# Kernel tuning notes

Measured on AMD Instinct MI355X. Metric: run time of the kernel, lower is better.

Reference implementation:

```python
import jax, jax.numpy as jnp
import numpy as np

EPS = 1e-5

def _layernorm(x, gamma, beta):
    mu = jnp.mean(x, axis=-1, keepdims=True)
    var = jnp.var(x, axis=-1, keepdims=True)
    return (x - mu) * jax.lax.rsqrt(var + EPS) * gamma + beta

def setup_inputs() -> dict:
    key = jax.random.key(0)
    ks = jax.random.split(key, 8)
    B, N, c_z, c_h = 1, 384, 128, 128
    s_z = 1.0 / np.sqrt(c_z)
    s_h = 1.0 / np.sqrt(c_h)
    return {
        "z_ij": jax.random.normal(ks[0], (B, N, N, c_z), dtype=jnp.float32),
        "ln_in_g": jnp.ones((c_z,), jnp.float32),
        "ln_in_b": jnp.zeros((c_z,), jnp.float32),
        "ln_out_g": jnp.ones((c_h,), jnp.float32),
        "ln_out_b": jnp.zeros((c_h,), jnp.float32),
        "Wa1": jax.random.uniform(ks[1], (c_h, c_z), jnp.float32, -s_z, s_z),
        "Wa2": jax.random.uniform(ks[2], (c_h, c_z), jnp.float32, -s_z, s_z),
        "Wb1": jax.random.uniform(ks[3], (c_h, c_z), jnp.float32, -s_z, s_z),
        "Wb2": jax.random.uniform(ks[4], (c_h, c_z), jnp.float32, -s_z, s_z),
        "Wg": jax.random.uniform(ks[5], (c_z, c_z), jnp.float32, -s_z, s_z),
        "Wout": jax.random.uniform(ks[6], (c_z, c_h), jnp.float32, -s_h, s_h),
    }

def reference(z_ij, ln_in_g, ln_in_b, ln_out_g, ln_out_b, Wa1, Wa2, Wb1, Wb2, Wg, Wout):
    # Algorithm 12: triangular multiplicative update, "outgoing" edges
    z = _layernorm(z_ij, ln_in_g, ln_in_b)              # [B,N,N,c_z]
    a = jax.nn.sigmoid(z @ Wa1.T) * (z @ Wa2.T)         # [B,N,N,c_h]
    b = jax.nn.sigmoid(z @ Wb1.T) * (z @ Wb2.T)         # [B,N,N,c_h]
    g = jax.nn.sigmoid(z @ Wg.T)                        # [B,N,N,c_z]
    s = jnp.einsum('bikd,bjkd->bijd', a, b)             # pairwise contraction over k
    return g * (_layernorm(s, ln_out_g, ln_out_b) @ Wout.T)
```

## Files before the change

kernel.cpp:

```cpp
#include <hip/hip_runtime.h>
#include <stdint.h>

#define N 384
#define NR (N*N)
#define PL (NR + 64)
#define C 128
#define WSZ 16384

typedef unsigned short ushort_t;
typedef __attribute__((ext_vector_type(8))) _Float16 f16x8;
typedef __attribute__((ext_vector_type(4))) float f32x4;

__device__ __forceinline__ ushort_t f2h(float f) {
  union { _Float16 h; ushort_t u; } v; v.h = (_Float16)f; return v.u;
}
__device__ __forceinline__ float h2f(ushort_t u) {
  union { _Float16 h; ushort_t u; } v; v.u = u; return (float)v.h;
}
__device__ __forceinline__ void unpack8h(uint4 q, float f[8]) {
  union { uint4 q; _Float16 h[8]; } v; v.q = q;
#pragma unroll
  for (int e = 0; e < 8; ++e) f[e] = (float)v.h[e];
}
__device__ __forceinline__ uint4 pack8h(const float f[8]) {
  union { uint4 q; _Float16 h[8]; } v;
#pragma unroll
  for (int e = 0; e < 8; ++e) v.h[e] = (_Float16)f[e];
  return v.q;
}

__device__ __forceinline__ float bf2f(ushort_t u) {
  union { unsigned int i; float f; } v; v.i = ((unsigned int)u) << 16; return v.f;
}
__device__ __forceinline__ ushort_t f2bf(float f) {
  union { float f; unsigned int i; } v; v.f = f;
  unsigned int u = v.i + 0x7FFF + ((v.i >> 16) & 1);
  return (ushort_t)(u >> 16);
}
__device__ __forceinline__ void unpack8bf(uint4 q, float f[8]) {
  const unsigned int* w = (const unsigned int*)&q;
#pragma unroll
  for (int e = 0; e < 4; ++e) {
    f[2*e]   = bf2f((ushort_t)(w[e] & 0xffffu));
    f[2*e+1] = bf2f((ushort_t)(w[e] >> 16));
  }
}
__device__ __forceinline__ uint4 pack8bf(const float f[8]) {
  uint4 q;
  unsigned int* w = (unsigned int*)&q;
#pragma unroll
  for (int e = 0; e < 4; ++e)
    w[e] = (unsigned int)f2bf(f[2*e]) | ((unsigned int)f2bf(f[2*e+1]) << 16);
  return q;
}

__device__ __forceinline__ float sigmoidf_(float x) {
  return __builtin_amdgcn_rcpf(1.0f + __expf(-x));
}

__device__ __forceinline__ void load8f(const void* p, size_t idx, int isf32, float f[8]) {
  if (isf32) {
    const float* q = (const float*)p + idx;
    const float4 a = ((const float4*)q)[0];
    const float4 b = ((const float4*)q)[1];
    f[0]=a.x; f[1]=a.y; f[2]=a.z; f[3]=a.w;
    f[4]=b.x; f[5]=b.y; f[6]=b.z; f[7]=b.w;
  } else {
    unpack8bf(*(const uint4*)((const ushort_t*)p + idx), f);
  }
}
__device__ __forceinline__ void store8(void* p, size_t idx, int isf32, const float f[8]) {
  if (isf32) {
    float* q = (float*)p + idx;
    ((float4*)q)[0] = make_float4(f[0], f[1], f[2], f[3]);
    ((float4*)q)[1] = make_float4(f[4], f[5], f[6], f[7]);
  } else {
    *(uint4*)((ushort_t*)p + idx) = pack8bf(f);
  }
}
__device__ __forceinline__ void store1(void* p, size_t idx, int isf32, float v) {
  if (isf32) ((float*)p)[idx] = v;
  else       ((ushort_t*)p)[idx] = f2bf(v);
}

__global__ void kprep(const unsigned int* __restrict__ zw,
                      const void* __restrict__ Wa1, const void* __restrict__ Wa2,
                      const void* __restrict__ Wb1, const void* __restrict__ Wb2,
                      const void* __restrict__ Wg,  const void* __restrict__ Wout,
                      ushort_t* __restrict__ wp, int* __restrict__ flag)
{
  const int t = threadIdx.x;
  __shared__ int cnt[4];
  {
    unsigned int u = zw[t];
    int e = (u >> 23) & 0xFF;
    int sane = (e >= 87 && e <= 132) ? 1 : 0;
    unsigned long long b = __ballot(sane);
    if ((t & 63) == 0) cnt[t >> 6] = __popcll(b);
  }
  __syncthreads();
  const int isf32 = ((cnt[0] + cnt[1] + cnt[2] + cnt[3]) >= 128) ? 1 : 0;
  if (blockIdx.x == 0 && t == 0) flag[0] = isf32;

  const void* src;
  switch (blockIdx.x) {
    case 0: src = Wa1; break;
    case 1: src = Wa2; break;
    case 2: src = Wb1; break;
    case 3: src = Wb2; break;
    case 4: src = Wg;  break;
    default: src = Wout; break;
  }
  ushort_t* dst = wp + (size_t)blockIdx.x * WSZ;
  for (int c = t; c < 2048; c += 256) {
    int ks = c >> 9, nf = (c >> 6) & 7, lane = c & 63;
    int quad = lane >> 4, l16 = lane & 15;
    size_t sidx = (size_t)(nf*16 + l16)*128 + ks*32 + quad*8;
    float f[8]; load8f(src, sidx, isf32, f);
    *(uint4*)(dst + (size_t)c*8) = pack8h(f);
  }
}

__global__ __launch_bounds__(256, 2)
void k1(const void* __restrict__ z, const void* __restrict__ gin,
        const void* __restrict__ bin, const ushort_t* __restrict__ wp,
        ushort_t* __restrict__ a_t, ushort_t* __restrict__ b_t,
        void* __restrict__ gout, ushort_t* __restrict__ g_t, int gIsWs,
        const int* __restrict__ flag)
{
  __shared__ ushort_t tb[128*72];
  const int t = threadIdx.x;
  const int isf32 = *flag;
  const int wave = t >> 6, lane = t & 63;
  const int quad = lane >> 4, l16 = lane & 15;
  const int rg = wave >> 1, ch = wave & 1;
  const int R0 = blockIdx.x * 64;
  const f32x4 z4 = {0.f, 0.f, 0.f, 0.f};

  f16x8 af[2][4];
#pragma unroll
  for (int mf = 0; mf < 2; ++mf) {
    const int row = R0 + rg*32 + mf*16 + l16;
    f16x8 xh[4];
    float s = 0.f, q = 0.f;
#pragma unroll
    for (int ks = 0; ks < 4; ++ks) {
      float x[8];
      load8f(z, (size_t)row*C + ks*32 + quad*8, isf32, x);
      union { _Float16 h[8]; f16x8 v; } u;
#pragma unroll
      for (int e = 0; e < 8; ++e) {
        s += x[e]; q += x[e]*x[e];
        u.h[e] = (_Float16)x[e];
      }
      xh[ks] = u.v;
    }
    s += __shfl_xor(s, 16); s += __shfl_xor(s, 32);
    q += __shfl_xor(q, 16); q += __shfl_xor(q, 32);
    const float mu = s * 0.0078125f;
    const float rstd = rsqrtf(q * 0.0078125f - mu*mu + 1e-5f);
#pragma unroll
    for (int ks = 0; ks < 4; ++ks) {
      float ga[8], be[8];
      load8f(gin, (size_t)(ks*32 + quad*8), isf32, ga);
      load8f(bin, (size_t)(ks*32 + quad*8), isf32, be);
      union { _Float16 h[8]; f16x8 v; } xi; xi.v = xh[ks];
      union { alignas(16) _Float16 h[8]; f16x8 v; } u;
#pragma unroll
      for (int e = 0; e < 8; ++e)
        u.h[e] = (_Float16)(((float)xi.h[e] - mu) * rstd * ga[e] + be[e]);
      af[mf][ks] = u.v;
    }
  }

  auto pair = [&](const ushort_t* W1p, const ushort_t* W2p, ushort_t* dst) {
#pragma unroll 1
    for (int nh = 0; nh < 2; ++nh) {
      f32x4 a1[2][2], a2[2][2];
#pragma unroll
      for (int mf = 0; mf < 2; ++mf)
#pragma unroll
        for (int nn = 0; nn < 2; ++nn) { a1[mf][nn] = z4; a2[mf][nn] = z4; }
#pragma unroll
      for (int ks = 0; ks < 4; ++ks)
#pragma unroll
        for (int nn = 0; nn < 2; ++nn) {
          const size_t foff = (size_t)((ks*8 + ch*4 + nh*2 + nn)*64 + lane) * 8;
          f16x8 b1 = *(const f16x8*)(W1p + foff);
          f16x8 b2 = *(const f16x8*)(W2p + foff);
#pragma unroll
          for (int mf = 0; mf < 2; ++mf) {
            a1[mf][nn] = __builtin_amdgcn_mfma_f32_16x16x32_f16(af[mf][ks], b1, a1[mf][nn], 0, 0, 0);
            a2[mf][nn] = __builtin_amdgcn_mfma_f32_16x16x32_f16(af[mf][ks], b2, a2[mf][nn], 0, 0, 0);
          }
        }
#pragma unroll
      for (int mf = 0; mf < 2; ++mf)
#pragma unroll
        for (int nn = 0; nn < 2; ++nn)
#pragma unroll
          for (int r = 0; r < 4; ++r) {
            int rowl = rg*32 + mf*16 + quad*4 + r;
            int col  = ch*64 + (nh*2 + nn)*16 + l16;
            tb[col*72 + rowl] = f2h(a2[mf][nn][r] * sigmoidf_(a1[mf][nn][r]));
          }
    }
    asm volatile("s_waitcnt lgkmcnt(0)" ::: "memory");
    __builtin_amdgcn_s_barrier();
#pragma unroll
    for (int i = 0; i < 4; ++i) {
      int cid = t + i*256, dl = cid >> 3, rc = cid & 7;
      uint4 v = *(const uint4*)(tb + dl*72 + rc*8);
      *(uint4*)(dst + (size_t)dl*PL + R0 + rc*8) = v;
    }
    asm volatile("" ::: "memory");
    __builtin_amdgcn_s_barrier();
  };
  pair(wp + 0*WSZ, wp + 1*WSZ, a_t);
  pair(wp + 2*WSZ, wp + 3*WSZ, b_t);

  {
    const ushort_t* Wgp = wp + 4*WSZ;
    f32x4 ag[2][4];
#pragma unroll
    for (int mf = 0; mf < 2; ++mf)
#pragma unroll
      for (int nf = 0; nf < 4; ++nf) ag[mf][nf] = z4;
#pragma unroll
    for (int ks = 0; ks < 4; ++ks)
#pragma unroll
      for (int nf = 0; nf < 4; ++nf) {
        const size_t foff = (size_t)((ks*8 + ch*4 + nf)*64 + lane) * 8;
        f16x8 b = *(const f16x8*)(Wgp + foff);
#pragma unroll
        for (int mf = 0; mf < 2; ++mf)
          ag[mf][nf] = __builtin_amdgcn_mfma_f32_16x16x32_f16(af[mf][ks], b, ag[mf][nf], 0, 0, 0);
      }
#pragma unroll
    for (int mf = 0; mf < 2; ++mf)
#pragma unroll
      for (int nf = 0; nf < 4; ++nf)
#pragma unroll
        for (int r = 0; r < 4; ++r) {
          int row = R0 + rg*32 + mf*16 + quad*4 + r;
          int col = ch*64 + nf*16 + l16;
          float v = sigmoidf_(ag[mf][nf][r]);
          size_t idx = (size_t)row*C + col;
          if (gIsWs) g_t[idx] = f2h(v);
          else       store1(gout, idx, isf32, v);
        }
  }
}

__global__ __launch_bounds__(256, 3)
void k2(const ushort_t* __restrict__ a_t, const ushort_t* __restrict__ b_t,
        ushort_t* __restrict__ s_t)
{
  __shared__ ushort_t As[128*64];
  __shared__ ushort_t Bs[128*64];
  const int t = threadIdx.x;
  const int wave = t >> 6, lane = t & 63;
  const int quad = lane >> 4, l16 = lane & 15;
  const int wm = wave >> 1, wn = wave & 1;
  const int lin = blockIdx.x;
  const int xcd = lin & 7, slot = lin >> 3;
  const int d = xcd + 8*(slot/9);
  const int tile = slot - (slot/9)*9;
  const int i0 = (tile/3) * 128, j0 = (tile%3) * 128;
  const size_t dbase = (size_t)d * PL;

  f32x4 acc[4][4];
  const f32x4 z4 = {0.f, 0.f, 0.f, 0.f};
#pragma unroll
  for (int mf = 0; mf < 4; ++mf)
#pragma unroll
    for (int nf = 0; nf < 4; ++nf) acc[mf][nf] = z4;

  uint4 va[4], vb[4];
#pragma unroll
  for (int j = 0; j < 4; ++j) {
    int cid = t + j*256, row = cid >> 3, c = cid & 7;
    va[j] = *(const uint4*)(a_t + dbase + (size_t)(i0 + row)*N + c*8);
    vb[j] = *(const uint4*)(b_t + dbase + (size_t)(j0 + row)*N + c*8);
  }

  for (int kt = 0; kt < 6; ++kt) {
#pragma unroll
    for (int j = 0; j < 4; ++j) {
      int cid = t + j*256, row = cid >> 3, c = cid & 7;
      int p = c ^ (row & 7);
      *(uint4*)(As + row*64 + p*8) = va[j];
      *(uint4*)(Bs + row*64 + p*8) = vb[j];
    }
    if (kt < 5) {
#pragma unroll
      for (int j = 0; j < 4; ++j) {
        int cid = t + j*256, row = cid >> 3, c = cid & 7;
        va[j] = *(const uint4*)(a_t + dbase + (size_t)(i0 + row)*N + (kt+1)*64 + c*8);
        vb[j] = *(const uint4*)(b_t + dbase + (size_t)(j0 + row)*N + (kt+1)*64 + c*8);
      }
    }
    asm volatile("s_waitcnt lgkmcnt(0)" ::: "memory");
    __builtin_amdgcn_s_barrier();

#pragma unroll
    for (int ks = 0; ks < 2; ++ks) {
      f16x8 af[4], bfr[4];
#pragma unroll
      for (int f = 0; f < 4; ++f) {
        int ra = wm*64 + f*16 + l16;
        int pa = (ks*4 + quad) ^ (ra & 7);
        af[f] = *(const f16x8*)(As + ra*64 + pa*8);
        int rb = wn*64 + f*16 + l16;
        int pb = (ks*4 + quad) ^ (rb & 7);
        bfr[f] = *(const f16x8*)(Bs + rb*64 + pb*8);
      }
#pragma unroll
      for (int mf = 0; mf < 4; ++mf)
#pragma unroll
        for (int nf = 0; nf < 4; ++nf)
          acc[mf][nf] = __builtin_amdgcn_mfma_f32_16x16x32_f16(af[mf], bfr[nf], acc[mf][nf], 0, 0, 0);
    }
    asm volatile("" ::: "memory");
    __builtin_amdgcn_s_barrier();
  }
#pragma unroll
  for (int mf = 0; mf < 4; ++mf)
#pragma unroll
    for (int nf = 0; nf < 4; ++nf)
#pragma unroll
      for (int r = 0; r < 4; ++r) {
        int row = wm*64 + mf*16 + quad*4 + r;
        int col = wn*64 + nf*16 + l16;
        s_t[dbase + (size_t)(i0 + row)*N + j0 + col] = f2h(acc[mf][nf][r]);
      }
}

__global__ __launch_bounds__(256, 2)
void k3(const ushort_t* __restrict__ s_t, const void* __restrict__ gno,
        const void* __restrict__ bno, const ushort_t* __restrict__ wp,
        void* __restrict__ io, const ushort_t* __restrict__ g_t, int gIsWs,
        const int* __restrict__ flag)
{
  __shared__ ushort_t ss[128*136];
  const int t = threadIdx.x;
  const int isf32 = *flag;
  const int wave = t >> 6, lane = t & 63;
  const int quad = lane >> 4, l16 = lane & 15;
  const int R0 = blockIdx.x * 128;
  const ushort_t* Woutp = wp + 5*WSZ;

  {
    const int dg = t >> 4, rg = t & 15;
    const int d0 = dg * 8;
    uint4 v[8];
#pragma unroll
    for (int dd = 0; dd < 8; ++dd)
      v[dd] = *(const uint4*)(s_t + (size_t)(d0 + dd)*PL + R0 + rg*8);
    const ushort_t* sv = (const ushort_t*)v;
#pragma unroll
    for (int rr0 = 0; rr0 < 8; ++rr0) {
      int rr = (rr0 + (t & 7)) & 7;
      ushort_t w[8];
#pragma unroll
      for (int dd = 0; dd < 8; ++dd) w[dd] = sv[dd*8 + rr];
      *(uint4*)(ss + (rg*8 + rr)*136 + d0) = *(const uint4*)w;
    }
  }
  asm volatile("s_waitcnt lgkmcnt(0)" ::: "memory");
  __builtin_amdgcn_s_barrier();

  {
    const int r = t >> 1, h = t & 1;
    float sum = 0.f, sq = 0.f;
#pragma unroll
    for (int j = 0; j < 8; ++j) {
      uint4 q = *(const uint4*)(ss + r*136 + (h*8 + j)*8);
      float f[8]; unpack8h(q, f);
#pragma unroll
      for (int e = 0; e < 8; ++e) { sum += f[e]; sq += f[e]*f[e]; }
    }
    sum += __shfl_xor(sum, 1);
    sq  += __shfl_xor(sq, 1);
    const float mu = sum * 0.0078125f;
    const float rstd = rsqrtf(sq * 0.0078125f - mu*mu + 1e-5f);
#pragma unroll
    for (int j = 0; j < 8; ++j) {
      const int g = h*8 + j;
      uint4 q = *(const uint4*)(ss + r*136 + g*8);
      float f[8], gm[8], bt[8];
      unpack8h(q, f);
      load8f(gno, (size_t)g*8, isf32, gm);
      load8f(bno, (size_t)g*8, isf32, bt);
#pragma unroll
      for (int e = 0; e < 8; ++e) f[e] = (f[e] - mu) * rstd * gm[e] + bt[e];
      *(uint4*)(ss + r*136 + g*8) = pack8h(f);
    }
  }
  asm volatile("s_waitcnt lgkmcnt(0)" ::: "memory");
  __builtin_amdgcn_s_barrier();

  f16x8 afr[2][4];
#pragma unroll
  for (int ks = 0; ks < 4; ++ks)
#pragma unroll
    for (int mf = 0; mf < 2; ++mf) {
      int row = wave*32 + mf*16 + l16;
      afr[mf][ks] = *(const f16x8*)(ss + row*136 + (ks*4 + quad)*8);
    }
  asm volatile("s_waitcnt lgkmcnt(0)" ::: "memory");
  __builtin_amdgcn_s_barrier();

  const f32x4 z4 = {0.f, 0.f, 0.f, 0.f};
#pragma unroll 1
  for (int nh = 0; nh < 2; ++nh) {
    f32x4 acc[2][4];
#pragma unroll
    for (int mf = 0; mf < 2; ++mf)
#pragma unroll
      for (int nn = 0; nn < 4; ++nn) acc[mf][nn] = z4;
#pragma unroll
    for (int ks = 0; ks < 4; ++ks)
#pragma unroll
      for (int nn = 0; nn < 4; ++nn) {
        size_t foff = (size_t)(((ks*8 + nh*4 + nn)*64 + lane)) * 8;
        f16x8 b = *(const f16x8*)(Woutp + foff);
#pragma unroll
        for (int mf = 0; mf < 2; ++mf)
          acc[mf][nn] = __builtin_amdgcn_mfma_f32_16x16x32_f16(afr[mf][ks], b, acc[mf][nn], 0, 0, 0);
      }
#pragma unroll
    for (int mf = 0; mf < 2; ++mf)
#pragma unroll
      for (int nn = 0; nn < 4; ++nn)
#pragma unroll
        for (int r = 0; r < 4; ++r) {
          int row = wave*32 + mf*16 + quad*4 + r;
          int col = (nh*4 + nn)*16 + l16;
          ss[row*136 + col] = f2h(acc[mf][nn][r]);
        }
  }
  asm volatile("s_waitcnt lgkmcnt(0)" ::: "memory");
  __builtin_amdgcn_s_barrier();

#pragma unroll
  for (int i = 0; i < 8; ++i) {
    int cid = t + i*256;
    int row = cid >> 4, ch = cid & 15;
    size_t idx = (size_t)(R0 + row)*C + ch*8;
    float gf[8], hf[8], of[8];
    if (gIsWs) unpack8h(*(const uint4*)(g_t + idx), gf);
    else       load8f(io, idx, isf32, gf);
    unpack8h(*(const uint4*)(ss + row*136 + ch*8), hf);
#pragma unroll
    for (int e = 0; e < 8; ++e) of[e] = gf[e] * hf[e];
    store8(io, idx, isf32, of);
  }
}

extern "C" void kernel_launch(void* const* d_in, const int* in_sizes, int n_in,
                              void* d_out, int out_size, void* d_ws, size_t ws_size,
                              hipStream_t stream) {
  (void)in_sizes; (void)n_in; (void)out_size;
  const void* z    = d_in[0];
  const void* gin  = d_in[1];
  const void* bin  = d_in[2];
  const void* gno  = d_in[3];
  const void* bno  = d_in[4];
  const void* Wa1  = d_in[5];
  const void* Wa2  = d_in[6];
  const void* Wb1  = d_in[7];
  const void* Wb2  = d_in[8];
  const void* Wg   = d_in[9];
  const void* Wout = d_in[10];

  const size_t plane = (size_t)C * PL;
  int* flag     = (int*)d_ws;
  ushort_t* wp  = (ushort_t*)((char*)d_ws + 256);
  ushort_t* a_t = wp + (size_t)6*WSZ;
  ushort_t* b_t = a_t + plane;
  ushort_t* s_t = b_t + plane;
  ushort_t* g_t = s_t + plane;
  size_t need_g = 256 + (size_t)6*WSZ*2 + (3*plane + (size_t)NR*C)*2;
  int gIsWs = (ws_size >= need_g) ? 1 : 0;

  kprep<<<6, 256, 0, stream>>>((const unsigned int*)z, Wa1, Wa2, Wb1, Wb2, Wg, Wout, wp, flag);
  k1<<<NR/64, 256, 0, stream>>>(z, gin, bin, wp, a_t, b_t, d_out, g_t, gIsWs, flag);
  k2<<<1152, 256, 0, stream>>>(a_t, b_t, s_t);
  k3<<<NR/128, 256, 0, stream>>>(s_t, gno, bno, wp, d_out, g_t, gIsWs, flag);
}
```

Measured before the change: 323.9 us.

## Double-buffer LDS in pairwise GEMM and cut register pressure in projection kernel

The contraction kernel now keeps two LDS buffers for the A and B tiles, so the next k-tile is written to the other buffer while MFMAs run on the current one. This removes one barrier per k-iteration. The doubled shared memory forces the occupancy hint down from 3 to 2 blocks per CU. In the projection kernel, the fp16 copy of the input row is no longer held in registers; the input is re-read from global memory to normalize it, which also avoids an extra fp16 rounding before normalization. The gate and pair GEMMs now loop over one output fragment at a time, shrinking the live accumulator set.

```diff
diff --git a/kernel.cpp b/kernel.cpp
--- a/kernel.cpp
+++ b/kernel.cpp
@@ -141,19 +141,13 @@
 #pragma unroll
   for (int mf = 0; mf < 2; ++mf) {
     const int row = R0 + rg*32 + mf*16 + l16;
-    f16x8 xh[4];
     float s = 0.f, q = 0.f;
 #pragma unroll
     for (int ks = 0; ks < 4; ++ks) {
       float x[8];
       load8f(z, (size_t)row*C + ks*32 + quad*8, isf32, x);
-      union { _Float16 h[8]; f16x8 v; } u;
-#pragma unroll
-      for (int e = 0; e < 8; ++e) {
-        s += x[e]; q += x[e]*x[e];
-        u.h[e] = (_Float16)x[e];
-      }
-      xh[ks] = u.v;
+#pragma unroll
+      for (int e = 0; e < 8; ++e) { s += x[e]; q += x[e]*x[e]; }
     }
     s += __shfl_xor(s, 16); s += __shfl_xor(s, 32);
     q += __shfl_xor(q, 16); q += __shfl_xor(q, 32);
@@ -161,49 +155,42 @@
     const float rstd = rsqrtf(q * 0.0078125f - mu*mu + 1e-5f);
 #pragma unroll
     for (int ks = 0; ks < 4; ++ks) {
-      float ga[8], be[8];
+      float x[8], ga[8], be[8];
+      load8f(z, (size_t)row*C + ks*32 + quad*8, isf32, x);
       load8f(gin, (size_t)(ks*32 + quad*8), isf32, ga);
       load8f(bin, (size_t)(ks*32 + quad*8), isf32, be);
-      union { _Float16 h[8]; f16x8 v; } xi; xi.v = xh[ks];
       union { alignas(16) _Float16 h[8]; f16x8 v; } u;
 #pragma unroll
       for (int e = 0; e < 8; ++e)
-        u.h[e] = (_Float16)(((float)xi.h[e] - mu) * rstd * ga[e] + be[e]);
+        u.h[e] = (_Float16)((x[e] - mu) * rstd * ga[e] + be[e]);
       af[mf][ks] = u.v;
     }
   }
 
   auto pair = [&](const ushort_t* W1p, const ushort_t* W2p, ushort_t* dst) {
 #pragma unroll 1
-    for (int nh = 0; nh < 2; ++nh) {
-      f32x4 a1[2][2], a2[2][2];
+    for (int nf = 0; nf < 4; ++nf) {
+      f32x4 a1[2], a2[2];
+      a1[0] = z4; a1[1] = z4; a2[0] = z4; a2[1] = z4;
+#pragma unroll
+      for (int ks = 0; ks < 4; ++ks) {
+        const size_t foff = (size_t)((ks*8 + ch*4 + nf)*64 + lane) * 8;
+        f16x8 b1 = *(const f16x8*)(W1p + foff);
+        f16x8 b2 = *(const f16x8*)(W2p + foff);
+#pragma unroll
+        for (int mf = 0; mf < 2; ++mf) {
+          a1[mf] = __builtin_amdgcn_mfma_f32_16x16x32_f16(af[mf][ks], b1, a1[mf], 0, 0, 0);
+          a2[mf] = __builtin_amdgcn_mfma_f32_16x16x32_f16(af[mf][ks], b2, a2[mf], 0, 0, 0);
+        }
+      }
 #pragma unroll
       for (int mf = 0; mf < 2; ++mf)
 #pragma unroll
-        for (int nn = 0; nn < 2; ++nn) { a1[mf][nn] = z4; a2[mf][nn] = z4; }
-#pragma unroll
-      for (int ks = 0; ks < 4; ++ks)
-#pragma unroll
-        for (int nn = 0; nn < 2; ++nn) {
-          const size_t foff = (size_t)((ks*8 + ch*4 + nh*2 + nn)*64 + lane) * 8;
-          f16x8 b1 = *(const f16x8*)(W1p + foff);
-          f16x8 b2 = *(const f16x8*)(W2p + foff);
-#pragma unroll
-          for (int mf = 0; mf < 2; ++mf) {
-            a1[mf][nn] = __builtin_amdgcn_mfma_f32_16x16x32_f16(af[mf][ks], b1, a1[mf][nn], 0, 0, 0);
-            a2[mf][nn] = __builtin_amdgcn_mfma_f32_16x16x32_f16(af[mf][ks], b2, a2[mf][nn], 0, 0, 0);
-          }
+        for (int r = 0; r < 4; ++r) {
+          int rowl = rg*32 + mf*16 + quad*4 + r;
+          int col  = ch*64 + nf*16 + l16;
+          tb[col*72 + rowl] = f2h(a2[mf][r] * sigmoidf_(a1[mf][r]));
         }
-#pragma unroll
-      for (int mf = 0; mf < 2; ++mf)
-#pragma unroll
-        for (int nn = 0; nn < 2; ++nn)
-#pragma unroll
-          for (int r = 0; r < 4; ++r) {
-            int rowl = rg*32 + mf*16 + quad*4 + r;
-            int col  = ch*64 + (nh*2 + nn)*16 + l16;
-            tb[col*72 + rowl] = f2h(a2[mf][nn][r] * sigmoidf_(a1[mf][nn][r]));
-          }
     }
     asm volatile("s_waitcnt lgkmcnt(0)" ::: "memory");
     __builtin_amdgcn_s_barrier();
@@ -221,43 +208,39 @@
 
   {
     const ushort_t* Wgp = wp + 4*WSZ;
-    f32x4 ag[2][4];
-#pragma unroll
-    for (int mf = 0; mf < 2; ++mf)
-#pragma unroll
-      for (int nf = 0; nf < 4; ++nf) ag[mf][nf] = z4;
-#pragma unroll
-    for (int ks = 0; ks < 4; ++ks)
-#pragma unroll
-      for (int nf = 0; nf < 4; ++nf) {
+#pragma unroll 1
+    for (int nf = 0; nf < 4; ++nf) {
+      f32x4 ag[2];
+      ag[0] = z4; ag[1] = z4;
+#pragma unroll
+      for (int ks = 0; ks < 4; ++ks) {
         const size_t foff = (size_t)((ks*8 + ch*4 + nf)*64 + lane) * 8;
         f16x8 b = *(const f16x8*)(Wgp + foff);
 #pragma unroll
         for (int mf = 0; mf < 2; ++mf)
-          ag[mf][nf] = __builtin_amdgcn_mfma_f32_16x16x32_f16(af[mf][ks], b, ag[mf][nf], 0, 0, 0);
-      }
-#pragma unroll
-    for (int mf = 0; mf < 2; ++mf)
-#pragma unroll
-      for (int nf = 0; nf < 4; ++nf)
+          ag[mf] = __builtin_amdgcn_mfma_f32_16x16x32_f16(af[mf][ks], b, ag[mf], 0, 0, 0);
+      }
+#pragma unroll
+      for (int mf = 0; mf < 2; ++mf)
 #pragma unroll
         for (int r = 0; r < 4; ++r) {
           int row = R0 + rg*32 + mf*16 + quad*4 + r;
           int col = ch*64 + nf*16 + l16;
-          float v = sigmoidf_(ag[mf][nf][r]);
+          float v = sigmoidf_(ag[mf][r]);
           size_t idx = (size_t)row*C + col;
           if (gIsWs) g_t[idx] = f2h(v);
           else       store1(gout, idx, isf32, v);
         }
-  }
-}
-
-__global__ __launch_bounds__(256, 3)
+    }
+  }
+}
+
+__global__ __launch_bounds__(256, 2)
 void k2(const ushort_t* __restrict__ a_t, const ushort_t* __restrict__ b_t,
         ushort_t* __restrict__ s_t)
 {
-  __shared__ ushort_t As[128*64];
-  __shared__ ushort_t Bs[128*64];
+  __shared__ ushort_t As[2][128*64];
+  __shared__ ushort_t Bs[2][128*64];
   const int t = threadIdx.x;
   const int wave = t >> 6, lane = t & 63;
   const int quad = lane >> 4, l16 = lane & 15;
@@ -283,46 +266,65 @@
     va[j] = *(const uint4*)(a_t + dbase + (size_t)(i0 + row)*N + c*8);
     vb[j] = *(const uint4*)(b_t + dbase + (size_t)(j0 + row)*N + c*8);
   }
+#pragma unroll
+  for (int j = 0; j < 4; ++j) {
+    int cid = t + j*256, row = cid >> 3, c = cid & 7;
+    int p = c ^ (row & 7);
+    *(uint4*)(&As[0][0] + row*64 + p*8) = va[j];
+    *(uint4*)(&Bs[0][0] + row*64 + p*8) = vb[j];
+  }
+#pragma unroll
+  for (int j = 0; j < 4; ++j) {
+    int cid = t + j*256, row = cid >> 3, c = cid & 7;
+    va[j] = *(const uint4*)(a_t + dbase + (size_t)(i0 + row)*N + 64 + c*8);
+    vb[j] = *(const uint4*)(b_t + dbase + (size_t)(j0 + row)*N + 64 + c*8);
+  }
+  asm volatile("s_waitcnt lgkmcnt(0)" ::: "memory");
+  __builtin_amdgcn_s_barrier();
 
   for (int kt = 0; kt < 6; ++kt) {
-#pragma unroll
-    for (int j = 0; j < 4; ++j) {
-      int cid = t + j*256, row = cid >> 3, c = cid & 7;
-      int p = c ^ (row & 7);
-      *(uint4*)(As + row*64 + p*8) = va[j];
-      *(uint4*)(Bs + row*64 + p*8) = vb[j];
-    }
-    if (kt < 5) {
-#pragma unroll
-      for (int j = 0; j < 4; ++j) {
-        int cid = t + j*256, row = cid >> 3, c = cid & 7;
-        va[j] = *(const uint4*)(a_t + dbase + (size_t)(i0 + row)*N + (kt+1)*64 + c*8);
-        vb[j] = *(const uint4*)(b_t + dbase + (size_t)(j0 + row)*N + (kt+1)*64 + c*8);
-      }
-    }
-    asm volatile("s_waitcnt lgkmcnt(0)" ::: "memory");
-    __builtin_amdgcn_s_barrier();
-
+    const int cur = kt & 1;
+    const ushort_t* Ab = &As[cur][0];
+    const ushort_t* Bb = &Bs[cur][0];
 #pragma unroll
     for (int ks = 0; ks < 2; ++ks) {
-      f16x8 af[4], bfr[4];
+      f16x8 afr[4], bfr[4];
 #pragma unroll
       for (int f = 0; f < 4; ++f) {
         int ra = wm*64 + f*16 + l16;
         int pa = (ks*4 + quad) ^ (ra & 7);
-        af[f] = *(const f16x8*)(As + ra*64 + pa*8);
+        afr[f] = *(const f16x8*)(Ab + ra*64 + pa*8);
         int rb = wn*64 + f*16 + l16;
         int pb = (ks*4 + quad) ^ (rb & 7);
-        bfr[f] = *(const f16x8*)(Bs + rb*64 + pb*8);
+        bfr[f] = *(const f16x8*)(Bb + rb*64 + pb*8);
       }
 #pragma unroll
       for (int mf = 0; mf < 4; ++mf)
 #pragma unroll
         for (int nf = 0; nf < 4; ++nf)
-          acc[mf][nf] = __builtin_amdgcn_mfma_f32_16x16x32_f16(af[mf], bfr[nf], acc[mf][nf], 0, 0, 0);
-    }
-    asm volatile("" ::: "memory");
-    __builtin_amdgcn_s_barrier();
+          acc[mf][nf] = __builtin_amdgcn_mfma_f32_16x16x32_f16(afr[mf], bfr[nf], acc[mf][nf], 0, 0, 0);
+    }
+    if (kt < 5) {
+      ushort_t* Aw = &As[cur ^ 1][0];
+      ushort_t* Bw = &Bs[cur ^ 1][0];
+#pragma unroll
+      for (int j = 0; j < 4; ++j) {
+        int cid = t + j*256, row = cid >> 3, c = cid & 7;
+        int p = c ^ (row & 7);
+        *(uint4*)(Aw + row*64 + p*8) = va[j];
+        *(uint4*)(Bw + row*64 + p*8) = vb[j];
+      }
+      if (kt < 4) {
+#pragma unroll
+        for (int j = 0; j < 4; ++j) {
+          int cid = t + j*256, row = cid >> 3, c = cid & 7;
+          va[j] = *(const uint4*)(a_t + dbase + (size_t)(i0 + row)*N + (kt+2)*64 + c*8);
+          vb[j] = *(const uint4*)(b_t + dbase + (size_t)(j0 + row)*N + (kt+2)*64 + c*8);
+        }
+      }
+      asm volatile("s_waitcnt lgkmcnt(0)" ::: "memory");
+      __builtin_amdgcn_s_barrier();
+    }
   }
 #pragma unroll
   for (int mf = 0; mf < 4; ++mf)
```

Measured after the change: 374.0 us. +15.5%, slower.
